# Performance work log

Measured on AMD Instinct MI355X. Metric: run time of the kernel, lower is better.

Reference implementation:

```python
import jax, jax.numpy as jnp
import numpy as np
import math

B, S, H = 8, 4096, 1024
E, I, K = 8, 2048, 2
CAP_FACTOR = 1.0


def setup_inputs() -> dict:
    key = jax.random.key(0)
    k1, k2, k3, k4 = jax.random.split(key, 4)
    # kaiming_uniform (linear): bound = sqrt(3 / fan_in), fan_in = last dim
    def kaiming(k, shape):
        bound = math.sqrt(3.0 / shape[-1])
        return jax.random.uniform(k, shape, jnp.float32, -bound, bound)
    x = jax.random.normal(k1, (B, S, H), jnp.float32)
    expert_embeddings = kaiming(k2, (E, H))
    first_linear = kaiming(k3, (E, I, H))
    second_linear = kaiming(k4, (E, H, I))
    return {"x": x, "expert_embeddings": expert_embeddings,
            "first_linear": first_linear, "second_linear": second_linear}


def _router(x, expert_embeddings):
    # dot: [B, S, E]
    dot = jnp.einsum('bsh,eh->bse', x, expert_embeddings)
    n = dot.shape[0] * dot.shape[1]
    dot2 = dot.reshape(n, E)
    vals, idx = jax.lax.top_k(dot2, K)                       # [N, K]
    rows = jnp.arange(n)[:, None]
    masked = jnp.full_like(dot2, -jnp.inf).at[rows, idx].set(vals)
    return jax.nn.softmax(masked, axis=-1)                   # [N, E]


def reference(x, expert_embeddings, first_linear, second_linear):
    batch, seq, hidden = x.shape
    n_tokens = batch * seq
    expert_capacity = math.ceil(n_tokens / E * CAP_FACTOR)

    weights = _router(x, expert_embeddings)                  # [N, E]
    ones = (weights > 0).astype(weights.dtype)               # tokens routed to expert
    # capacity mask: keep first expert_capacity tokens (in token order) per expert
    cap_ones = jnp.where(jnp.cumsum(ones, axis=0) <= expert_capacity, ones, 0.0)
    caw = weights * cap_ones                                 # [N, E]

    # topk over token dim per expert -> selected token slots
    vals, idx = jax.lax.top_k(caw.T, expert_capacity)        # [E, C]
    index = idx.reshape(-1)                                  # [E*C]

    x_flat = x.reshape(n_tokens, hidden)
    tokens = x_flat[index].reshape(E, expert_capacity, hidden)   # gather

    inter = jax.nn.relu(jnp.einsum('ech,eih->eci', tokens, first_linear))
    out = jnp.einsum('eci,ehi->ech', inter, second_linear)
    out = out * vals[:, :, None]                             # weight by router prob

    final = jnp.zeros((n_tokens, hidden), x.dtype).at[index].add(
        out.reshape(-1, hidden))                             # scatter-add combine
    return final.reshape(x.shape)
```

## Files before the change

kernel.cpp:

```cpp
#include <hip/hip_runtime.h>
#include <stdint.h>

#define N_TOK 32768
#define HID   1024
#define NE    8
#define NI    2048
#define CAP   4096

typedef short s16x8 __attribute__((ext_vector_type(8)));
typedef float f32x4 __attribute__((ext_vector_type(4)));

__device__ __forceinline__ unsigned short f2bf(float f) {
    unsigned int u = __builtin_bit_cast(unsigned int, f);
    u += 0x7fffu + ((u >> 16) & 1u);
    return (unsigned short)(u >> 16);
}

__device__ __forceinline__ void gload16(const void* g, void* l) {
    __builtin_amdgcn_global_load_lds(
        (const __attribute__((address_space(1))) unsigned int*)(uintptr_t)g,
        (__attribute__((address_space(3))) unsigned int*)(unsigned int)(uintptr_t)l,
        16, 0, 0);
}

#define WAIT_LGKM0 asm volatile("s_waitcnt lgkmcnt(0)" ::: "memory")
#define WAIT_VM6   asm volatile("s_waitcnt vmcnt(6)" ::: "memory")
#define WAIT_VM0   asm volatile("s_waitcnt vmcnt(0)" ::: "memory")
#define SFENCE     __builtin_amdgcn_sched_barrier(0)
#define BARR       __builtin_amdgcn_s_barrier()

#define STAGE(Ms, rM, tile, h) do { \
    unsigned short* _d = Ms + (((tile) & 1) * 16384) + (h) * 8192 + wave * 1024; \
    gload16(rM[h][0] + (tile) * 64 + gsl8, _d); \
    gload16(rM[h][1] + (tile) * 64 + gsl8, _d + 512); } while (0)

#define MFMA_CL(AF, BF, NB) do { \
    __builtin_amdgcn_s_setprio(1); \
    _Pragma("unroll") \
    for (int mi = 0; mi < 4; ++mi) \
    _Pragma("unroll") \
    for (int nj = 0; nj < 4; ++nj) \
        acc[mi][(NB) + nj] = __builtin_amdgcn_mfma_f32_16x16x32_bf16( \
            AF[mi], BF[(NB) + nj], acc[mi][(NB) + nj], 0, 0, 0); \
    __builtin_amdgcn_s_setprio(0); \
} while (0)

#define RD_A(DST, PH) do { \
    _Pragma("unroll") \
    for (int mi = 0; mi < 4; ++mi) \
        DST[mi] = *(const s16x8*)(As + buf + abase + mi * 1024 + (PH)); \
} while (0)

#define RD_B(DST, PH, NB) do { \
    _Pragma("unroll") \
    for (int nj = 0; nj < 4; ++nj) \
        DST[(NB) + nj] = *(const s16x8*)(Bs + buf + bbase + ((NB) + nj) * 1024 + (PH)); \
} while (0)

__global__ __launch_bounds__(256) void cvt_kernel(
    const float* __restrict__ src, unsigned short* __restrict__ dst, size_t n8)
{
    size_t i = (size_t)blockIdx.x * 256 + threadIdx.x;
    size_t stride = (size_t)gridDim.x * 256;
    for (; i < n8; i += stride) {
        float4 a0 = ((const float4*)src)[2 * i];
        float4 a1 = ((const float4*)src)[2 * i + 1];
        uint4 p;
        p.x = f2bf(a0.x) | ((unsigned)f2bf(a0.y) << 16);
        p.y = f2bf(a0.z) | ((unsigned)f2bf(a0.w) << 16);
        p.z = f2bf(a1.x) | ((unsigned)f2bf(a1.y) << 16);
        p.w = f2bf(a1.z) | ((unsigned)f2bf(a1.w) << 16);
        ((uint4*)dst)[i] = p;
    }
}

__global__ __launch_bounds__(256) void router_kernel(
    const float* __restrict__ x, const float* __restrict__ emb,
    int2* __restrict__ r_e, float2* __restrict__ r_w,
    unsigned short* __restrict__ xb)
{
    int token = blockIdx.x * 4 + (threadIdx.x >> 6);
    int lane  = threadIdx.x & 63;
    const float4* xr = (const float4*)(x + (size_t)token * HID);
    const float4* er = (const float4*)emb;

    float a[NE];
#pragma unroll
    for (int e = 0; e < NE; ++e) a[e] = 0.f;
    uint2 pk[4];
#pragma unroll
    for (int j = 0; j < 4; ++j) {
        float4 v = xr[j * 64 + lane];
        pk[j].x = f2bf(v.x) | ((unsigned)f2bf(v.y) << 16);
        pk[j].y = f2bf(v.z) | ((unsigned)f2bf(v.w) << 16);
#pragma unroll
        for (int e = 0; e < NE; ++e) {
            float4 w = er[e * 256 + j * 64 + lane];
            a[e] += v.x * w.x + v.y * w.y + v.z * w.z + v.w * w.w;
        }
    }
    uint2* xbr = (uint2*)(xb + (size_t)token * HID);
#pragma unroll
    for (int j = 0; j < 4; ++j) xbr[j * 64 + lane] = pk[j];

#pragma unroll
    for (int e = 0; e < NE; ++e) {
        for (int off = 32; off; off >>= 1) a[e] += __shfl_xor(a[e], off);
    }
    if (lane == 0) {
        float v1 = -1e30f, v2 = -1e30f; int i1 = 0, i2 = 0;
#pragma unroll
        for (int e = 0; e < NE; ++e) {
            float v = a[e];
            if (v > v1) { v2 = v1; i2 = i1; v1 = v; i1 = e; }
            else if (v > v2) { v2 = v; i2 = e; }
        }
        float ex = __expf(v2 - v1);
        r_e[token] = make_int2(i1, i2);
        r_w[token] = make_float2(1.f / (1.f + ex), ex / (1.f + ex));
    }
}

__global__ __launch_bounds__(1024) void count_kernel(
    const int2* __restrict__ r_e, int* __restrict__ bc)
{
    __shared__ int cnt[NE];
    if (threadIdx.x < NE) cnt[threadIdx.x] = 0;
    __syncthreads();
    int n = blockIdx.x * 1024 + threadIdx.x;
    int2 e = r_e[n];
    atomicAdd(&cnt[e.x], 1);
    atomicAdd(&cnt[e.y], 1);
    __syncthreads();
    if (threadIdx.x < NE) bc[blockIdx.x * NE + threadIdx.x] = cnt[threadIdx.x];
}

__global__ void prefix_kernel(const int* __restrict__ bc, int* __restrict__ bb)
{
    int e = threadIdx.x;
    if (e >= NE) return;
    int run = 0;
    for (int b = 0; b < N_TOK / 1024; ++b) {
        bb[b * NE + e] = run;
        run += bc[b * NE + e];
    }
}

__global__ __launch_bounds__(1024) void assign_kernel(
    const int2* __restrict__ r_e, const float2* __restrict__ r_w,
    const int* __restrict__ bb,
    int* __restrict__ tok_list, float* __restrict__ w_list)
{
    __shared__ int wavecnt[16][NE];
    __shared__ int waveoff[16][NE];
    int tid = threadIdx.x, lane = tid & 63, wv = tid >> 6;
    int n = blockIdx.x * 1024 + tid;
    int2 e = r_e[n];
    float2 w = r_w[n];
    unsigned long long below = (1ull << lane) - 1ull;
    int rank0 = 0, rank1 = 0;
#pragma unroll
    for (int ex = 0; ex < NE; ++ex) {
        unsigned long long m = __ballot(e.x == ex || e.y == ex);
        if (lane == 0) wavecnt[wv][ex] = __popcll(m);
        int r = __popcll(m & below);
        if (e.x == ex) rank0 = r;
        if (e.y == ex) rank1 = r;
    }
    __syncthreads();
    if (tid < NE) {
        int run = 0;
        for (int w2 = 0; w2 < 16; ++w2) { waveoff[w2][tid] = run; run += wavecnt[w2][tid]; }
    }
    __syncthreads();
    int s0 = bb[blockIdx.x * NE + e.x] + waveoff[wv][e.x] + rank0;
    int s1 = bb[blockIdx.x * NE + e.y] + waveoff[wv][e.y] + rank1;
    if (s0 < CAP) { tok_list[e.x * CAP + s0] = n; w_list[e.x * CAP + s0] = w.x; }
    if (s1 < CAP) { tok_list[e.y * CAP + s1] = n; w_list[e.y * CAP + s1] = w.y; }
}

__global__ __launch_bounds__(512, 2) void gemm1_k(
    const unsigned short* __restrict__ xb,
    const unsigned short* __restrict__ w1b,
    const int* __restrict__ tok_list,
    unsigned short* __restrict__ inter,
    int eb)
{
    constexpr int K = HID, T = K / 64;
    __shared__ __align__(16) unsigned short smem[65536];
    unsigned short* As = smem;
    unsigned short* Bs = smem + 32768;

    const int nblk = gridDim.x;
    const int lin  = blockIdx.x;
    const int wg   = (lin & 7) * (nblk >> 3) + (lin >> 3);
    const int tn = wg & 7;
    const int tm = (wg >> 3) & 15;
    const int ez = wg >> 7;
    const int e  = eb + ez;

    const int tid = threadIdx.x, lane = tid & 63, wave = tid >> 6;
    const int wr = wave >> 1, wc = wave & 1;
    const int gsl8 = ((lane & 7) ^ (lane >> 3)) * 8;
    const int abase = (wr >> 1) * 8192 + (((wr & 1) * 64 + (lane & 15))) * 64;
    const int bbase = wc * 8192 + (lane & 15) * 64;
    const int ph0 = ((lane >> 4) ^ (lane & 7)) * 8;
    const int ph1 = ((4 + (lane >> 4)) ^ (lane & 7)) * 8;
    const int rbase = wave * 16 + (lane >> 3);

    const int* tl = tok_list + e * CAP + tm * 256;
    const unsigned short* rA[2][2];
    const unsigned short* rB[2][2];
#pragma unroll
    for (int h = 0; h < 2; ++h)
#pragma unroll
        for (int j = 0; j < 2; ++j) {
            rA[h][j] = xb + (size_t)tl[h * 128 + rbase + j * 8] * K;
            rB[h][j] = w1b + ((size_t)e * NI + tn * 256 + h * 128 + rbase + j * 8) * K;
        }

    f32x4 acc[4][8];
#pragma unroll
    for (int i = 0; i < 4; ++i)
#pragma unroll
        for (int j = 0; j < 8; ++j) acc[i][j] = (f32x4)0.f;

    s16x8 afr0[4], afr1[4], bfr0[8], bfr1[8];

    STAGE(As, rA, 0, 0); STAGE(As, rA, 0, 1);
    STAGE(Bs, rB, 0, 0); STAGE(Bs, rB, 0, 1);
    STAGE(As, rA, 1, 0);
    STAGE(Bs, rB, 1, 0); STAGE(Bs, rB, 1, 1);
    WAIT_VM6; SFENCE; BARR; SFENCE;

#pragma unroll 2
    for (int t = 0; t < T; ++t) {
        const int buf = (t & 1) * 16384;
        if (t + 1 < T) STAGE(As, rA, t + 1, 1);
        RD_A(afr0, ph0);
        RD_B(bfr0, ph0, 0);
        RD_B(bfr0, ph0, 4);
        MFMA_CL(afr0, bfr0, 0);
        RD_A(afr1, ph1);
        MFMA_CL(afr0, bfr0, 4);
        RD_B(bfr1, ph1, 0);
        RD_B(bfr1, ph1, 4);
        MFMA_CL(afr1, bfr1, 0);
        WAIT_LGKM0; SFENCE; BARR; SFENCE;
        if (t + 2 < T) { STAGE(As, rA, t + 2, 0); STAGE(Bs, rB, t + 2, 0); STAGE(Bs, rB, t + 2, 1); }
        MFMA_CL(afr1, bfr1, 4);
        if (t < T - 2) { WAIT_VM6; } else { WAIT_VM0; }
        SFENCE; BARR; SFENCE;
    }

    __syncthreads();
#pragma unroll
    for (int mi = 0; mi < 4; ++mi)
#pragma unroll
        for (int ni = 0; ni < 8; ++ni)
#pragma unroll
            for (int r = 0; r < 4; ++r) {
                int row = wr * 64 + mi * 16 + (lane >> 4) * 4 + r;
                int c   = wc * 128 + ni * 16 + (lane & 15);
                float v = acc[mi][ni][r];
                v = v > 0.f ? v : 0.f;
                smem[row * 256 + (((c >> 3) ^ (row & 7)) << 3) + (c & 7)] = f2bf(v);
            }
    __syncthreads();
    unsigned short* Cp = inter + ((size_t)ez * CAP + tm * 256) * NI + tn * 256;
#pragma unroll
    for (int it = 0; it < 16; ++it) {
        int v = tid + it * 512;
        int row = v >> 5, s = v & 31;
        uint4 val = *(const uint4*)&smem[row * 256 + ((s ^ (row & 7)) << 3)];
        *(uint4*)&Cp[(size_t)row * NI + s * 8] = val;
    }
}

__global__ __launch_bounds__(512, 2) void gemm2_k(
    const unsigned short* __restrict__ inter,
    const unsigned short* __restrict__ w2b,
    const int* __restrict__ tok_list,
    const float* __restrict__ w_list,
    float* __restrict__ out,
    int eb)
{
    constexpr int K = NI, T = K / 64;
    __shared__ __align__(16) unsigned short smem[65536];
    unsigned short* As = smem;
    unsigned short* Bs = smem + 32768;

    const int nblk = gridDim.x;
    const int lin  = blockIdx.x;
    const int wg   = (lin & 7) * (nblk >> 3) + (lin >> 3);
    const int tn = wg & 3;
    const int tm = (wg >> 2) & 15;
    const int ez = wg >> 6;
    const int e  = eb + ez;

    const int tid = threadIdx.x, lane = tid & 63, wave = tid >> 6;
    const int wr = wave >> 1, wc = wave & 1;
    const int gsl8 = ((lane & 7) ^ (lane >> 3)) * 8;
    const int abase = (wr >> 1) * 8192 + (((wr & 1) * 64 + (lane & 15))) * 64;
    const int bbase = wc * 8192 + (lane & 15) * 64;
    const int ph0 = ((lane >> 4) ^ (lane & 7)) * 8;
    const int ph1 = ((4 + (lane >> 4)) ^ (lane & 7)) * 8;
    const int rbase = wave * 16 + (lane >> 3);

    const unsigned short* rA[2][2];
    const unsigned short* rB[2][2];
#pragma unroll
    for (int h = 0; h < 2; ++h)
#pragma unroll
        for (int j = 0; j < 2; ++j) {
            rA[h][j] = inter + ((size_t)ez * CAP + tm * 256 + h * 128 + rbase + j * 8) * (size_t)K;
            rB[h][j] = w2b + ((size_t)e * HID + tn * 256 + h * 128 + rbase + j * 8) * (size_t)K;
        }

    f32x4 acc[4][8];
#pragma unroll
    for (int i = 0; i < 4; ++i)
#pragma unroll
        for (int j = 0; j < 8; ++j) acc[i][j] = (f32x4)0.f;

    s16x8 afr0[4], afr1[4], bfr0[8], bfr1[8];

    STAGE(As, rA, 0, 0); STAGE(As, rA, 0, 1);
    STAGE(Bs, rB, 0, 0); STAGE(Bs, rB, 0, 1);
    STAGE(As, rA, 1, 0);
    STAGE(Bs, rB, 1, 0); STAGE(Bs, rB, 1, 1);
    WAIT_VM6; SFENCE; BARR; SFENCE;

#pragma unroll 2
    for (int t = 0; t < T; ++t) {
        const int buf = (t & 1) * 16384;
        if (t + 1 < T) STAGE(As, rA, t + 1, 1);
        RD_A(afr0, ph0);
        RD_B(bfr0, ph0, 0);
        RD_B(bfr0, ph0, 4);
        MFMA_CL(afr0, bfr0, 0);
        RD_A(afr1, ph1);
        MFMA_CL(afr0, bfr0, 4);
        RD_B(bfr1, ph1, 0);
        RD_B(bfr1, ph1, 4);
        MFMA_CL(afr1, bfr1, 0);
        WAIT_LGKM0; SFENCE; BARR; SFENCE;
        if (t + 2 < T) { STAGE(As, rA, t + 2, 0); STAGE(Bs, rB, t + 2, 0); STAGE(Bs, rB, t + 2, 1); }
        MFMA_CL(afr1, bfr1, 4);
        if (t < T - 2) { WAIT_VM6; } else { WAIT_VM0; }
        SFENCE; BARR; SFENCE;
    }

    const int* tl   = tok_list + e * CAP + tm * 256;
    const float* wl = w_list  + e * CAP + tm * 256;
#pragma unroll
    for (int mi = 0; mi < 4; ++mi)
#pragma unroll
        for (int r = 0; r < 4; ++r) {
            int rrow = wr * 64 + mi * 16 + (lane >> 4) * 4 + r;
            int tok  = tl[rrow];
            float w  = wl[rrow];
            float* orow = out + (size_t)tok * HID + tn * 256 + wc * 128;
#pragma unroll
            for (int ni = 0; ni < 8; ++ni)
                atomicAdd(&orow[ni * 16 + (lane & 15)], acc[mi][ni][r] * w);
        }
}

extern "C" void kernel_launch(void* const* d_in, const int* in_sizes, int n_in,
                              void* d_out, int out_size, void* d_ws, size_t ws_size,
                              hipStream_t stream)
{
    const float* x   = (const float*)d_in[0];
    const float* emb = (const float*)d_in[1];
    const float* W1  = (const float*)d_in[2];
    const float* W2  = (const float*)d_in[3];
    float* out = (float*)d_out;

    size_t off = 0;
    auto alloc = [&](size_t bytes) -> void* {
        void* p = (char*)d_ws + off;
        off += (bytes + 255) & ~(size_t)255;
        return p;
    };
    const size_t sz_w  = (size_t)NE * NI * HID * 2;
    const size_t sz_xb = (size_t)N_TOK * HID * 2;

    int*   tok_list = (int*)alloc((size_t)NE * CAP * 4);
    float* w_list   = (float*)alloc((size_t)NE * CAP * 4);
    unsigned short* w1b = (unsigned short*)alloc(sz_w);
    unsigned short* w2b = (unsigned short*)alloc(sz_w);
    unsigned short* xb  = (unsigned short*)alloc(sz_xb);

    unsigned short* inter = (unsigned short*)((char*)d_ws + off);
    size_t avail = ws_size > off ? ws_size - off : 0;
    const size_t per_e = (size_t)CAP * NI * 2;
    int G = (avail >= 8 * per_e) ? 8 : (avail >= 4 * per_e) ? 4
          : (avail >= 2 * per_e) ? 2 : 1;

    int2*   r_e = (int2*)inter;
    float2* r_w = (float2*)((char*)inter + (size_t)N_TOK * 8);
    int*    bc  = (int*)((char*)inter + (size_t)N_TOK * 16);
    int*    bb  = bc + (N_TOK / 1024) * NE;

    hipMemsetAsync(d_out, 0, (size_t)N_TOK * HID * 4, stream);
    hipMemsetAsync(tok_list, 0, (size_t)NE * CAP * 4, stream);
    hipMemsetAsync(w_list, 0, (size_t)NE * CAP * 4, stream);

    cvt_kernel<<<2048, 256, 0, stream>>>(W1, w1b, (size_t)NE * NI * HID / 8);
    cvt_kernel<<<2048, 256, 0, stream>>>(W2, w2b, (size_t)NE * HID * NI / 8);
    router_kernel<<<N_TOK / 4, 256, 0, stream>>>(x, emb, r_e, r_w, xb);
    count_kernel<<<N_TOK / 1024, 1024, 0, stream>>>(r_e, bc);
    prefix_kernel<<<1, 64, 0, stream>>>(bc, bb);
    assign_kernel<<<N_TOK / 1024, 1024, 0, stream>>>(r_e, r_w, bb, tok_list, w_list);

    for (int eb = 0; eb < NE; eb += G) {
        gemm1_k<<<dim3(8 * 16 * G), 512, 0, stream>>>(xb, w1b, tok_list, inter, eb);
        gemm2_k<<<dim3(4 * 16 * G), 512, 0, stream>>>(inter, w2b, tok_list, w_list, out, eb);
    }
}
```

Measured before the change: 472.9 us.

## Replace 256x256 pipelined GEMM tiles with simple single-buffered 128x128 tiles

Both expert GEMMs drop the hand-scheduled 256x256 tile with 512 threads, double buffering, explicit waitcnt and setprio. They now use 128x128 tiles with 256 threads, one LDS buffer and two __syncthreads per K step. The smaller tiles and smaller LDS footprint allow more blocks per CU and a larger grid, but global loads no longer overlap with MFMA work, and each element is reused less, so L2 traffic rises.

Measured after the change: 516.8 us. +9.3%, slower.

```diff
diff --git a/kernel.cpp b/kernel.cpp
--- a/kernel.cpp
+++ b/kernel.cpp
@@ -22,40 +22,6 @@
         (__attribute__((address_space(3))) unsigned int*)(unsigned int)(uintptr_t)l,
         16, 0, 0);
 }
-
-#define WAIT_LGKM0 asm volatile("s_waitcnt lgkmcnt(0)" ::: "memory")
-#define WAIT_VM6   asm volatile("s_waitcnt vmcnt(6)" ::: "memory")
-#define WAIT_VM0   asm volatile("s_waitcnt vmcnt(0)" ::: "memory")
-#define SFENCE     __builtin_amdgcn_sched_barrier(0)
-#define BARR       __builtin_amdgcn_s_barrier()
-
-#define STAGE(Ms, rM, tile, h) do { \
-    unsigned short* _d = Ms + (((tile) & 1) * 16384) + (h) * 8192 + wave * 1024; \
-    gload16(rM[h][0] + (tile) * 64 + gsl8, _d); \
-    gload16(rM[h][1] + (tile) * 64 + gsl8, _d + 512); } while (0)
-
-#define MFMA_CL(AF, BF, NB) do { \
-    __builtin_amdgcn_s_setprio(1); \
-    _Pragma("unroll") \
-    for (int mi = 0; mi < 4; ++mi) \
-    _Pragma("unroll") \
-    for (int nj = 0; nj < 4; ++nj) \
-        acc[mi][(NB) + nj] = __builtin_amdgcn_mfma_f32_16x16x32_bf16( \
-            AF[mi], BF[(NB) + nj], acc[mi][(NB) + nj], 0, 0, 0); \
-    __builtin_amdgcn_s_setprio(0); \
-} while (0)
-
-#define RD_A(DST, PH) do { \
-    _Pragma("unroll") \
-    for (int mi = 0; mi < 4; ++mi) \
-        DST[mi] = *(const s16x8*)(As + buf + abase + mi * 1024 + (PH)); \
-} while (0)
-
-#define RD_B(DST, PH, NB) do { \
-    _Pragma("unroll") \
-    for (int nj = 0; nj < 4; ++nj) \
-        DST[(NB) + nj] = *(const s16x8*)(Bs + buf + bbase + ((NB) + nj) * 1024 + (PH)); \
-} while (0)
 
 __global__ __launch_bounds__(256) void cvt_kernel(
     const float* __restrict__ src, unsigned short* __restrict__ dst, size_t n8)
@@ -179,7 +145,8 @@
     if (s1 < CAP) { tok_list[e.y * CAP + s1] = n; w_list[e.y * CAP + s1] = w.y; }
 }
 
-__global__ __launch_bounds__(512, 2) void gemm1_k(
+
+__global__ __launch_bounds__(256, 3) void gemm1_k(
     const unsigned short* __restrict__ xb,
     const unsigned short* __restrict__ w1b,
     const int* __restrict__ tok_list,
@@ -187,97 +154,93 @@
     int eb)
 {
     constexpr int K = HID, T = K / 64;
-    __shared__ __align__(16) unsigned short smem[65536];
+    __shared__ __align__(16) unsigned short smem[32768];
     unsigned short* As = smem;
-    unsigned short* Bs = smem + 32768;
+    unsigned short* Bs = smem + 8192;
 
     const int nblk = gridDim.x;
     const int lin  = blockIdx.x;
     const int wg   = (lin & 7) * (nblk >> 3) + (lin >> 3);
-    const int tn = wg & 7;
-    const int tm = (wg >> 3) & 15;
-    const int ez = wg >> 7;
+    const int tn = wg & 15;
+    const int tm = (wg >> 4) & 31;
+    const int ez = wg >> 9;
     const int e  = eb + ez;
 
     const int tid = threadIdx.x, lane = tid & 63, wave = tid >> 6;
     const int wr = wave >> 1, wc = wave & 1;
-    const int gsl8 = ((lane & 7) ^ (lane >> 3)) * 8;
-    const int abase = (wr >> 1) * 8192 + (((wr & 1) * 64 + (lane & 15))) * 64;
-    const int bbase = wc * 8192 + (lane & 15) * 64;
-    const int ph0 = ((lane >> 4) ^ (lane & 7)) * 8;
-    const int ph1 = ((4 + (lane >> 4)) ^ (lane & 7)) * 8;
-    const int rbase = wave * 16 + (lane >> 3);
-
-    const int* tl = tok_list + e * CAP + tm * 256;
-    const unsigned short* rA[2][2];
-    const unsigned short* rB[2][2];
-#pragma unroll
-    for (int h = 0; h < 2; ++h)
-#pragma unroll
-        for (int j = 0; j < 2; ++j) {
-            rA[h][j] = xb + (size_t)tl[h * 128 + rbase + j * 8] * K;
-            rB[h][j] = w1b + ((size_t)e * NI + tn * 256 + h * 128 + rbase + j * 8) * K;
-        }
-
-    f32x4 acc[4][8];
+    const int gsl8 = ((lane & 7) ^ ((lane >> 3) & 7)) * 8;
+    const int abase = (wr * 64 + (lane & 15)) * 64;
+    const int bbase = (wc * 64 + (lane & 15)) * 64;
+    const int phs[2] = { (((lane >> 4)) ^ (lane & 7)) * 8,
+                         ((4 + (lane >> 4)) ^ (lane & 7)) * 8 };
+
+    const int* tl = tok_list + e * CAP + tm * 128;
+    const unsigned short* srcA[4];
+    const unsigned short* srcB[4];
+#pragma unroll
+    for (int c = 0; c < 4; ++c) {
+        int row = c * 32 + wave * 8 + (lane >> 3);
+        srcA[c] = xb + (size_t)tl[row] * K + gsl8;
+        srcB[c] = w1b + ((size_t)e * NI + tn * 128 + row) * K + gsl8;
+    }
+
+    f32x4 acc[4][4];
 #pragma unroll
     for (int i = 0; i < 4; ++i)
 #pragma unroll
-        for (int j = 0; j < 8; ++j) acc[i][j] = (f32x4)0.f;
-
-    s16x8 afr0[4], afr1[4], bfr0[8], bfr1[8];
-
-    STAGE(As, rA, 0, 0); STAGE(As, rA, 0, 1);
-    STAGE(Bs, rB, 0, 0); STAGE(Bs, rB, 0, 1);
-    STAGE(As, rA, 1, 0);
-    STAGE(Bs, rB, 1, 0); STAGE(Bs, rB, 1, 1);
-    WAIT_VM6; SFENCE; BARR; SFENCE;
-
-#pragma unroll 2
+        for (int j = 0; j < 4; ++j) acc[i][j] = (f32x4)0.f;
+
     for (int t = 0; t < T; ++t) {
-        const int buf = (t & 1) * 16384;
-        if (t + 1 < T) STAGE(As, rA, t + 1, 1);
-        RD_A(afr0, ph0);
-        RD_B(bfr0, ph0, 0);
-        RD_B(bfr0, ph0, 4);
-        MFMA_CL(afr0, bfr0, 0);
-        RD_A(afr1, ph1);
-        MFMA_CL(afr0, bfr0, 4);
-        RD_B(bfr1, ph1, 0);
-        RD_B(bfr1, ph1, 4);
-        MFMA_CL(afr1, bfr1, 0);
-        WAIT_LGKM0; SFENCE; BARR; SFENCE;
-        if (t + 2 < T) { STAGE(As, rA, t + 2, 0); STAGE(Bs, rB, t + 2, 0); STAGE(Bs, rB, t + 2, 1); }
-        MFMA_CL(afr1, bfr1, 4);
-        if (t < T - 2) { WAIT_VM6; } else { WAIT_VM0; }
-        SFENCE; BARR; SFENCE;
-    }
-
-    __syncthreads();
+#pragma unroll
+        for (int c = 0; c < 4; ++c) {
+            unsigned short* d = smem + (c * 32 + wave * 8) * 64;
+            gload16(srcA[c] + t * 64, d);
+            gload16(srcB[c] + t * 64, d + 8192);
+        }
+        __syncthreads();
+#pragma unroll
+        for (int ks = 0; ks < 2; ++ks) {
+            s16x8 af[4], bf[4];
+#pragma unroll
+            for (int mi = 0; mi < 4; ++mi)
+                af[mi] = *(const s16x8*)(As + abase + mi * 1024 + phs[ks]);
+#pragma unroll
+            for (int ni = 0; ni < 4; ++ni)
+                bf[ni] = *(const s16x8*)(Bs + bbase + ni * 1024 + phs[ks]);
+#pragma unroll
+            for (int mi = 0; mi < 4; ++mi)
+#pragma unroll
+                for (int ni = 0; ni < 4; ++ni)
+                    acc[mi][ni] = __builtin_amdgcn_mfma_f32_16x16x32_bf16(
+                        af[mi], bf[ni], acc[mi][ni], 0, 0, 0);
+        }
+        __syncthreads();
+    }
+
 #pragma unroll
     for (int mi = 0; mi < 4; ++mi)
 #pragma unroll
-        for (int ni = 0; ni < 8; ++ni)
+        for (int ni = 0; ni < 4; ++ni)
 #pragma unroll
             for (int r = 0; r < 4; ++r) {
                 int row = wr * 64 + mi * 16 + (lane >> 4) * 4 + r;
-                int c   = wc * 128 + ni * 16 + (lane & 15);
+                int c   = wc * 64 + ni * 16 + (lane & 15);
                 float v = acc[mi][ni][r];
                 v = v > 0.f ? v : 0.f;
-                smem[row * 256 + (((c >> 3) ^ (row & 7)) << 3) + (c & 7)] = f2bf(v);
+                smem[row * 128 + (((c >> 3) ^ (row & 7)) << 3) + (c & 7)] = f2bf(v);
             }
     __syncthreads();
-    unsigned short* Cp = inter + ((size_t)ez * CAP + tm * 256) * NI + tn * 256;
-#pragma unroll
-    for (int it = 0; it < 16; ++it) {
-        int v = tid + it * 512;
-        int row = v >> 5, s = v & 31;
-        uint4 val = *(const uint4*)&smem[row * 256 + ((s ^ (row & 7)) << 3)];
+    unsigned short* Cp = inter + ((size_t)ez * CAP + tm * 128) * NI + tn * 128;
+#pragma unroll
+    for (int it = 0; it < 8; ++it) {
+        int v = tid + it * 256;
+        int row = v >> 4, s = v & 15;
+        uint4 val = *(const uint4*)&smem[row * 128 + ((s ^ (row & 7)) << 3)];
         *(uint4*)&Cp[(size_t)row * NI + s * 8] = val;
     }
 }
 
-__global__ __launch_bounds__(512, 2) void gemm2_k(
+__global__ __launch_bounds__(256, 3) void gemm2_k(
     const unsigned short* __restrict__ inter,
     const unsigned short* __restrict__ w2b,
     const int* __restrict__ tok_list,
@@ -286,73 +249,70 @@
     int eb)
 {
     constexpr int K = NI, T = K / 64;
-    __shared__ __align__(16) unsigned short smem[65536];
+    __shared__ __align__(16) unsigned short smem[16384];
     unsigned short* As = smem;
-    unsigned short* Bs = smem + 32768;
+    unsigned short* Bs = smem + 8192;
 
     const int nblk = gridDim.x;
     const int lin  = blockIdx.x;
     const int wg   = (lin & 7) * (nblk >> 3) + (lin >> 3);
-    const int tn = wg & 3;
-    const int tm = (wg >> 2) & 15;
-    const int ez = wg >> 6;
+    const int tn = wg & 7;
+    const int tm = (wg >> 3) & 31;
+    const int ez = wg >> 8;
     const int e  = eb + ez;
 
     const int tid = threadIdx.x, lane = tid & 63, wave = tid >> 6;
     const int wr = wave >> 1, wc = wave & 1;
-    const int gsl8 = ((lane & 7) ^ (lane >> 3)) * 8;
-    const int abase = (wr >> 1) * 8192 + (((wr & 1) * 64 + (lane & 15))) * 64;
-    const int bbase = wc * 8192 + (lane & 15) * 64;
-    const int ph0 = ((lane >> 4) ^ (lane & 7)) * 8;
-    const int ph1 = ((4 + (lane >> 4)) ^ (lane & 7)) * 8;
-    const int rbase = wave * 16 + (lane >> 3);
-
-    const unsigned short* rA[2][2];
-    const unsigned short* rB[2][2];
-#pragma unroll
-    for (int h = 0; h < 2; ++h)
-#pragma unroll
-        for (int j = 0; j < 2; ++j) {
-            rA[h][j] = inter + ((size_t)ez * CAP + tm * 256 + h * 128 + rbase + j * 8) * (size_t)K;
-            rB[h][j] = w2b + ((size_t)e * HID + tn * 256 + h * 128 + rbase + j * 8) * (size_t)K;
-        }
-
-    f32x4 acc[4][8];
+    const int gsl8 = ((lane & 7) ^ ((lane >> 3) & 7)) * 8;
+    const int abase = (wr * 64 + (lane & 15)) * 64;
+    const int bbase = (wc * 64 + (lane & 15)) * 64;
+    const int phs[2] = { (((lane >> 4)) ^ (lane & 7)) * 8,
+                         ((4 + (lane >> 4)) ^ (lane & 7)) * 8 };
+
+    const unsigned short* srcA[4];
+    const unsigned short* srcB[4];
+#pragma unroll
+    for (int c = 0; c < 4; ++c) {
+        int row = c * 32 + wave * 8 + (lane >> 3);
+        srcA[c] = inter + ((size_t)ez * CAP + tm * 128 + row) * (size_t)K + gsl8;
+        srcB[c] = w2b + ((size_t)e * HID + tn * 128 + row) * (size_t)K + gsl8;
+    }
+
+    f32x4 acc[4][4];
 #pragma unroll
     for (int i = 0; i < 4; ++i)
 #pragma unroll
-        for (int j = 0; j < 8; ++j) acc[i][j] = (f32x4)0.f;
-
-    s16x8 afr0[4], afr1[4], bfr0[8], bfr1[8];
-
-    STAGE(As, rA, 0, 0); STAGE(As, rA, 0, 1);
-    STAGE(Bs, rB, 0, 0); STAGE(Bs, rB, 0, 1);
-    STAGE(As, rA, 1, 0);
-    STAGE(Bs, rB, 1, 0); STAGE(Bs, rB, 1, 1);
-    WAIT_VM6; SFENCE; BARR; SFENCE;
-
-#pragma unroll 2
+        for (int j = 0; j < 4; ++j) acc[i][j] = (f32x4)0.f;
+
     for (int t = 0; t < T; ++t) {
-        const int buf = (t & 1) * 16384;
-        if (t + 1 < T) STAGE(As, rA, t + 1, 1);
-        RD_A(afr0, ph0);
-        RD_B(bfr0, ph0, 0);
-        RD_B(bfr0, ph0, 4);
-        MFMA_CL(afr0, bfr0, 0);
-        RD_A(afr1, ph1);
-        MFMA_CL(afr0, bfr0, 4);
-        RD_B(bfr1, ph1, 0);
-        RD_B(bfr1, ph1, 4);
-        MFMA_CL(afr1, bfr1, 0);
-        WAIT_LGKM0; SFENCE; BARR; SFENCE;
-        if (t + 2 < T) { STAGE(As, rA, t + 2, 0); STAGE(Bs, rB, t + 2, 0); STAGE(Bs, rB, t + 2, 1); }
-        MFMA_CL(afr1, bfr1, 4);
-        if (t < T - 2) { WAIT_VM6; } else { WAIT_VM0; }
-        SFENCE; BARR; SFENCE;
-    }
-
-    const int* tl   = tok_list + e * CAP + tm * 256;
-    const float* wl = w_list  + e * CAP + tm * 256;
+#pragma unroll
+        for (int c = 0; c < 4; ++c) {
+            unsigned short* d = smem + (c * 32 + wave * 8) * 64;
+            gload16(srcA[c] + t * 64, d);
+            gload16(srcB[c] + t * 64, d + 8192);
+        }
+        __syncthreads();
+#pragma unroll
+        for (int ks = 0; ks < 2; ++ks) {
+            s16x8 af[4], bf[4];
+#pragma unroll
+            for (int mi = 0; mi < 4; ++mi)
+                af[mi] = *(const s16x8*)(As + abase + mi * 1024 + phs[ks]);
+#pragma unroll
+            for (int ni = 0; ni < 4; ++ni)
+                bf[ni] = *(const s16x8*)(Bs + bbase + ni * 1024 + phs[ks]);
+#pragma unroll
+            for (int mi = 0; mi < 4; ++mi)
+#pragma unroll
+                for (int ni = 0; ni < 4; ++ni)
+                    acc[mi][ni] = __builtin_amdgcn_mfma_f32_16x16x32_bf16(
+                        af[mi], bf[ni], acc[mi][ni], 0, 0, 0);
+        }
+        __syncthreads();
+    }
+
+    const int* tl   = tok_list + e * CAP + tm * 128;
+    const float* wl = w_list  + e * CAP + tm * 128;
 #pragma unroll
     for (int mi = 0; mi < 4; ++mi)
 #pragma unroll
@@ -360,9 +320,9 @@
             int rrow = wr * 64 + mi * 16 + (lane >> 4) * 4 + r;
             int tok  = tl[rrow];
             float w  = wl[rrow];
-            float* orow = out + (size_t)tok * HID + tn * 256 + wc * 128;
-#pragma unroll
-            for (int ni = 0; ni < 8; ++ni)
+            float* orow = out + (size_t)tok * HID + tn * 128 + wc * 64;
+#pragma unroll
+            for (int ni = 0; ni < 4; ++ni)
                 atomicAdd(&orow[ni * 16 + (lane & 15)], acc[mi][ni][r] * w);
         }
 }
@@ -415,7 +375,7 @@
     assign_kernel<<<N_TOK / 1024, 1024, 0, stream>>>(r_e, r_w, bb, tok_list, w_list);
 
     for (int eb = 0; eb < NE; eb += G) {
-        gemm1_k<<<dim3(8 * 16 * G), 512, 0, stream>>>(xb, w1b, tok_list, inter, eb);
-        gemm2_k<<<dim3(4 * 16 * G), 512, 0, stream>>>(inter, w2b, tok_list, w_list, out, eb);
-    }
-}
+        gemm1_k<<<dim3(16 * 32 * G), 256, 0, stream>>>(xb, w1b, tok_list, inter, eb);
+        gemm2_k<<<dim3(8 * 32 * G), 256, 0, stream>>>(inter, w2b, tok_list, w_list, out, eb);
+    }
+}
```
